# Kernel tuning notes

Hardware: AMD Instinct MI355X
Metric: run time of the kernel (lower is better)

## Reference

```python
import jax, jax.numpy as jnp
import numpy as np

N_NODES = 100000
N_EDGES = 1600000
HIDDEN = 128
N_REL = 8


def setup_inputs() -> dict:
    key = jax.random.key(0)
    ks = jax.random.split(key, 12)
    s = 1.0 / np.sqrt(HIDDEN)
    inp = {
        "node_idx": jnp.arange(N_NODES, dtype=jnp.int32),
        "edge_index": jax.random.randint(ks[0], (2, N_EDGES), 0, N_NODES, dtype=jnp.int32),
        "edge_type": jax.random.randint(ks[1], (N_EDGES,), 0, N_REL, dtype=jnp.int32),
        "embedding": jax.random.normal(ks[2], (N_NODES, HIDDEN), jnp.float32),
        "W_rel_0": jax.random.normal(ks[3], (N_REL, HIDDEN, HIDDEN), jnp.float32) * s,
        "W_root_0": jax.random.normal(ks[4], (HIDDEN, HIDDEN), jnp.float32) * s,
        "b_0": jnp.zeros((HIDDEN,), jnp.float32),
        "W_rel_1": jax.random.normal(ks[5], (N_REL, HIDDEN, HIDDEN), jnp.float32) * s,
        "W_root_1": jax.random.normal(ks[6], (HIDDEN, HIDDEN), jnp.float32) * s,
        "b_1": jnp.zeros((HIDDEN,), jnp.float32),
    }
    return inp


def _rgcn_conv(x, src, dst, et, W_rel, W_root, b):
    # PyG RGCNConv: out_i = x_i @ W_root + b + sum_r mean_{j in N_r(i)} x_j @ W_r
    n = x.shape[0]
    r = W_rel.shape[0]
    # Transform all nodes by all relations once (R small), then gather per edge.
    x_all = jnp.einsum('nd,rdf->rnf', x, W_rel)          # [R, N, d]
    msg = x_all[et, src]                                  # [E, d]
    # per-(relation, dst) mean normalization
    seg = et * n + dst                                    # [E]
    deg = jax.ops.segment_sum(jnp.ones(et.shape, jnp.float32), seg, num_segments=r * n)
    norm = 1.0 / jnp.maximum(deg[seg], 1.0)               # [E]
    agg = jax.ops.segment_sum(msg * norm[:, None], dst, num_segments=n)  # [N, d]
    return agg + x @ W_root + b


def reference(node_idx, edge_index, edge_type, embedding,
              W_rel_0, W_root_0, b_0, W_rel_1, W_root_1, b_1):
    src, dst = edge_index[0], edge_index[1]
    x = embedding[node_idx]
    x = jax.nn.relu(_rgcn_conv(x, src, dst, edge_type, W_rel_0, W_root_0, b_0))
    x = jax.nn.relu(_rgcn_conv(x, src, dst, edge_type, W_rel_1, W_root_1, b_1))
    return x
```

## Files before the change

### kernel.cpp

```cpp
#include <hip/hip_runtime.h>
#include <hip/hip_bf16.h>

typedef short bf16x8 __attribute__((ext_vector_type(8)));
typedef float f32x4 __attribute__((ext_vector_type(4)));

constexpr int NN = 100000;
constexpr int NE = 1600000;
constexpr int HH = 128;
constexpr int NR = 8;
constexpr int NBIN = 782;
constexpr int CAPB = 6144;

__device__ __forceinline__ unsigned short f2bf(float f) {
    unsigned b = __float_as_uint(f);
    b += 0x7fffu + ((b >> 16) & 1u);
    return (unsigned short)(b >> 16);
}

__global__ void convertWX(const float* __restrict__ Wr0, const float* __restrict__ Wq0,
                          const float* __restrict__ Wr1, const float* __restrict__ Wq1,
                          unsigned short* __restrict__ Wt,
                          const int* __restrict__ node_idx,
                          const float* __restrict__ emb,
                          unsigned* __restrict__ xb32) {
    if (blockIdx.x < 1152) {
        int o = blockIdx.x * 256 + threadIdx.x;
        int L = o / 147456;
        int rem = o - L * 147456;
        int s = rem >> 14;
        int p = rem & 16383;
        int f = p >> 7;
        int d = p & 127;
        const float* Wq = L ? Wq1 : Wq0;
        const float* Wr = L ? Wr1 : Wr0;
        float v = (s == 0) ? Wq[d * 128 + f] : Wr[((s - 1) * 128 + d) * 128 + f];
        int cs = (d >> 3) ^ (f & 7);
        Wt[(o & ~127) | (cs << 3) | (d & 7)] = f2bf(v);
    } else {
        int i = (blockIdx.x - 1152) * 256 + threadIdx.x;
        if (i >= NN * 64) return;
        int n = i >> 6, dp = i & 63;
        int row = node_idx[n];
        float2 v = *((const float2*)(emb + (size_t)row * HH) + dp);
        xb32[(size_t)n * 64 + dp] = (unsigned)f2bf(v.x) | ((unsigned)f2bf(v.y) << 16);
    }
}

__global__ __launch_bounds__(256) void binCount(const int* __restrict__ edst,
                                                unsigned* __restrict__ binCounts) {
    __shared__ unsigned hist[NBIN];
    for (int i = threadIdx.x; i < NBIN; i += 256) hist[i] = 0;
    __syncthreads();
    int stride = gridDim.x * 256;
    for (int e = blockIdx.x * 256 + threadIdx.x; e < NE; e += stride)
        atomicAdd(&hist[((unsigned)edst[e]) >> 7], 1u);
    __syncthreads();
    for (int i = threadIdx.x; i < NBIN; i += 256)
        if (hist[i]) atomicAdd(&binCounts[i], hist[i]);
}

__global__ void binScan(const unsigned* __restrict__ binCounts,
                        unsigned* __restrict__ binStarts,
                        unsigned* __restrict__ binCursor) {
    __shared__ unsigned sh[1024];
    int tid = threadIdx.x;
    unsigned v = (tid < NBIN) ? binCounts[tid] : 0u;
    sh[tid] = v;
    __syncthreads();
    for (int ofs = 1; ofs < 1024; ofs <<= 1) {
        unsigned t = (tid >= ofs) ? sh[tid - ofs] : 0u;
        __syncthreads();
        sh[tid] += t;
        __syncthreads();
    }
    if (tid < NBIN) {
        unsigned s = sh[tid] - v;
        binStarts[tid] = s;
        binCursor[tid] = s;
    }
    if (tid == 0) binStarts[NBIN] = NE;
}

__global__ __launch_bounds__(256) void binScatter(
        const int* __restrict__ esrc, const int* __restrict__ edst,
        const int* __restrict__ etype, unsigned* __restrict__ binCursor,
        unsigned* __restrict__ binned) {
    __shared__ unsigned hist[NBIN];
    __shared__ unsigned cur[NBIN];
    for (int i = threadIdx.x; i < NBIN; i += 256) hist[i] = 0;
    __syncthreads();
    int per = (NE + gridDim.x - 1) / gridDim.x;
    int lo = blockIdx.x * per;
    int hi = lo + per; if (hi > NE) hi = NE;
    for (int e = lo + threadIdx.x; e < hi; e += 256)
        atomicAdd(&hist[((unsigned)edst[e]) >> 7], 1u);
    __syncthreads();
    for (int i = threadIdx.x; i < NBIN; i += 256) {
        unsigned c = hist[i];
        cur[i] = c ? atomicAdd(&binCursor[i], c) : 0u;
    }
    __syncthreads();
    for (int e = lo + threadIdx.x; e < hi; e += 256) {
        unsigned d = (unsigned)edst[e];
        unsigned b = d >> 7;
        unsigned pos = atomicAdd(&cur[b], 1u);
        binned[pos] = (unsigned)esrc[e] | (((unsigned)etype[e]) << 17) |
                      ((d & 127u) << 20);
    }
}

__global__ __launch_bounds__(256) void binSort(
        const unsigned* __restrict__ binStarts, const unsigned* __restrict__ binned,
        unsigned* __restrict__ epk, unsigned* __restrict__ starts) {
    __shared__ unsigned hist[1024];
    __shared__ unsigned scn[1024];
    __shared__ unsigned cnts[1024];
    __shared__ unsigned part[256];
    __shared__ unsigned buf[CAPB];
    __shared__ unsigned outb[CAPB];
    int bin = blockIdx.x;
    int tid = threadIdx.x;
    unsigned base = binStarts[bin];
    int cnt = (int)(binStarts[bin + 1] - base);

    for (int i = tid; i < 1024; i += 256) hist[i] = 0;
    __syncthreads();
    for (int i = tid; i < cnt; i += 256) {
        unsigned p = binned[base + i];
        if (i < CAPB) buf[i] = p;
        atomicAdd(&hist[(p >> 17) & 0x3ffu], 1u);
    }
    __syncthreads();
    unsigned h4[4], tsum = 0;
#pragma unroll
    for (int j = 0; j < 4; ++j) { h4[j] = hist[tid * 4 + j]; tsum += h4[j]; }
    part[tid] = tsum;
    __syncthreads();
    for (int ofs = 1; ofs < 256; ofs <<= 1) {
        unsigned t = (tid >= ofs) ? part[tid - ofs] : 0u;
        __syncthreads();
        part[tid] += t;
        __syncthreads();
    }
    unsigned run = part[tid] - tsum;
#pragma unroll
    for (int j = 0; j < 4; ++j) { scn[tid * 4 + j] = run; run += h4[j]; }
    __syncthreads();
    for (int i = tid; i < 1024; i += 256) {
        starts[(size_t)bin * 1024 + i] = base + scn[i];
        cnts[i] = hist[i];
        hist[i] = scn[i];
    }
    __syncthreads();
    if (cnt <= CAPB) {
        for (int i = tid; i < cnt; i += 256) {
            unsigned p = buf[i];
            unsigned key = (p >> 17) & 0x3ffu;
            unsigned pos = atomicAdd(&hist[key], 1u);
            unsigned deg = cnts[key]; if (deg > 4095u) deg = 4095u;
            outb[pos] = ((p & 0x1ffffu) << 3) | (key & 7u) | (deg << 20);
        }
        __syncthreads();
        for (int i = tid; i < cnt; i += 256) epk[base + i] = outb[i];
    } else {
        for (int i = tid; i < cnt; i += 256) {
            unsigned p = binned[base + i];
            unsigned key = (p >> 17) & 0x3ffu;
            unsigned pos = atomicAdd(&hist[key], 1u);
            unsigned deg = cnts[key]; if (deg > 4095u) deg = 4095u;
            epk[base + pos] = ((p & 0x1ffffu) << 3) | (key & 7u) | (deg << 20);
        }
    }
}

__global__ __launch_bounds__(512, 4) void bigGemm(const unsigned short* x,
                                                  const unsigned short* __restrict__ Wt,
                                                  unsigned* __restrict__ y32,
                                                  unsigned* root32) {
    typedef __attribute__((address_space(3))) unsigned lds_u32_t;
    typedef const __attribute__((address_space(1))) unsigned glb_u32_t;
    __shared__ __align__(16) unsigned short Bl[2][16384];
    __shared__ __align__(16) unsigned Tld[64 * 64];

    int tid = threadIdx.x;
    int wid = tid >> 6, lane = tid & 63;
    int quad = lane >> 4, l16 = lane & 15;
    int wr = wid >> 1, wc = wid & 1;
    int m0 = blockIdx.x * 128;
    int sw = l16 & 7;

    auto prefetch = [&](int s, int b) {
        const char* gs = (const char*)Wt + (size_t)s * 32768 + wid * 4096 + lane * 16;
        char* ls = (char*)&Bl[b][0] + wid * 4096;
#pragma unroll
        for (int j = 0; j < 4; ++j)
            __builtin_amdgcn_global_load_lds((glb_u32_t*)(const void*)(gs + j * 1024),
                                             (lds_u32_t*)(void*)(ls + j * 1024),
                                             16, 0, 0);
    };

    prefetch(0, 0);

    bf16x8 ax[2][4];
#pragma unroll
    for (int nt = 0; nt < 2; ++nt) {
        int node = m0 + wr * 32 + nt * 16 + l16;
        node = node < NN ? node : NN - 1;
        const unsigned short* rp = x + (size_t)node * HH + quad * 8;
#pragma unroll
        for (int kt = 0; kt < 4; ++kt)
            ax[nt][kt] = *(const bf16x8*)(rp + kt * 32);
    }
    __syncthreads();

    for (int s = 0; s < 9; ++s) {
        if (s < 8) prefetch(s + 1, (s + 1) & 1);
        const char* Bb = (const char*)&Bl[s & 1][0];

        f32x4 acc[2][4];
#pragma unroll
        for (int nt = 0; nt < 2; ++nt)
#pragma unroll
            for (int ft = 0; ft < 4; ++ft) acc[nt][ft] = (f32x4){0.f, 0.f, 0.f, 0.f};

#pragma unroll
        for (int kt = 0; kt < 4; ++kt) {
            bf16x8 bw[4];
#pragma unroll
            for (int ft = 0; ft < 4; ++ft) {
                int f = wc * 64 + ft * 16 + l16;
                bw[ft] = *(const bf16x8*)(Bb + f * 256 +
                                          (((kt * 4 + quad) ^ sw) << 4));
            }
#pragma unroll
            for (int nt = 0; nt < 2; ++nt)
#pragma unroll
                for (int ft = 0; ft < 4; ++ft)
                    acc[nt][ft] = __builtin_amdgcn_mfma_f32_16x16x32_bf16(
                        bw[ft], ax[nt][kt], acc[nt][ft], 0, 0, 0);
        }

#pragma unroll
        for (int h = 0; h < 2; ++h) {
            __syncthreads();
            if ((wr >> 1) == h) {
#pragma unroll
                for (int nt = 0; nt < 2; ++nt) {
                    int rT = (wr & 1) * 32 + nt * 16 + l16;
#pragma unroll
                    for (int ft = 0; ft < 4; ++ft) {
                        unsigned d0, d1;
                        asm("v_cvt_pk_bf16_f32 %0, %1, %2"
                            : "=v"(d0) : "v"(acc[nt][ft][0]), "v"(acc[nt][ft][1]));
                        asm("v_cvt_pk_bf16_f32 %0, %1, %2"
                            : "=v"(d1) : "v"(acc[nt][ft][2]), "v"(acc[nt][ft][3]));
                        int slot = wc * 16 + ft * 4 + quad;
                        *(uint2*)((char*)Tld + rT * 256 +
                                  ((slot ^ ((rT & 7) << 2)) << 3)) =
                            make_uint2(d0, d1);
                    }
                }
            }
            __syncthreads();
#pragma unroll
            for (int p = 0; p < 2; ++p) {
                int rT = p * 32 + wid * 4 + quad;
                uint4 v = *(const uint4*)((char*)Tld + rT * 256 +
                                          (((l16 * 2) ^ ((rT & 7) << 2)) << 3));
                int node = m0 + h * 64 + rT;
                if (node < NN) {
                    unsigned* dst = (s == 0) ? (root32 + (size_t)node * 64)
                                             : (y32 + ((size_t)node * 8 + (s - 1)) * 64);
                    *(uint4*)(dst + l16 * 4) = v;
                }
            }
        }
    }
}

__global__ __launch_bounds__(256) void scatterAgg(
        const unsigned* __restrict__ starts, const unsigned* __restrict__ epk,
        const unsigned* __restrict__ y32, const unsigned* root32,
        const float* __restrict__ bias,
        float* __restrict__ outF, unsigned* outB) {
    int node = blockIdx.x * 4 + (threadIdx.x >> 6);
    if (node >= NN) return;
    int lane = threadIdx.x & 63;

    unsigned s0 = starts[(size_t)node * 8];
    unsigned s1 = starts[(size_t)node * 8 + 8];
    int cnt = (int)__builtin_amdgcn_readfirstlane((int)(s1 - s0));

    float ax = 0.f, ay = 0.f;
    for (int c0 = 0; c0 < cnt; c0 += 64) {
        unsigned myE = s0 + (unsigned)c0 + (unsigned)lane;
        unsigned pk = (myE < s1) ? epk[myE] : 0u;
        int cend = cnt - c0;
        if (cend > 64) cend = 64;
        for (int base = 0; base < cend; base += 8) {
            int m = cend - base;
            if (m > 8) m = 8;
            int bix = base << 2;
            unsigned pj[8], qj[8];
#pragma unroll
            for (int j = 0; j < 8; ++j)
                pj[j] = (unsigned)__builtin_amdgcn_ds_bpermute(bix + (j << 2), (int)pk);
#pragma unroll
            for (int j = 0; j < 8; ++j)
                if (j < m) qj[j] = y32[((pj[j] & 0xFFFFFu) << 6) + (unsigned)lane];
#pragma unroll
            for (int j = 0; j < 8; ++j) {
                if (j < m) {
                    float nr = __builtin_amdgcn_rcpf((float)(pj[j] >> 20));
                    float lo = __uint_as_float(qj[j] << 16);
                    float hi = __uint_as_float(qj[j] & 0xffff0000u);
                    ax += lo * nr;
                    ay += hi * nr;
                }
            }
        }
    }

    unsigned r = root32[(size_t)node * 64 + lane];
    float2 bv = ((const float2*)bias)[lane];
    float ox = ax + __uint_as_float(r << 16) + bv.x;
    float oy = ay + __uint_as_float(r & 0xffff0000u) + bv.y;
    ox = ox > 0.f ? ox : 0.f;
    oy = oy > 0.f ? oy : 0.f;
    if (outF) {
        *(float2*)(outF + (size_t)node * HH + lane * 2) = make_float2(ox, oy);
    } else {
        outB[(size_t)node * 64 + lane] =
            (unsigned)f2bf(ox) | ((unsigned)f2bf(oy) << 16);
    }
}

extern "C" void kernel_launch(void* const* d_in, const int* in_sizes, int n_in,
                              void* d_out, int out_size, void* d_ws, size_t ws_size,
                              hipStream_t stream) {
    const int* node_idx = (const int*)d_in[0];
    const int* eidx     = (const int*)d_in[1];
    const int* etype    = (const int*)d_in[2];
    const float* emb    = (const float*)d_in[3];
    const float* Wr0    = (const float*)d_in[4];
    const float* Wq0    = (const float*)d_in[5];
    const float* b0     = (const float*)d_in[6];
    const float* Wr1    = (const float*)d_in[7];
    const float* Wq1    = (const float*)d_in[8];
    const float* b1     = (const float*)d_in[9];
    const int* esrc = eidx;
    const int* edst = eidx + NE;

    char* ws = (char*)d_ws;
    size_t off = 0;
    auto alloc = [&](size_t bytes) -> void* {
        void* p = ws + off;
        off = (off + bytes + 255) & ~(size_t)255;
        return p;
    };
    unsigned* binCounts = (unsigned*)alloc((size_t)NBIN * 4);
    unsigned* binStarts = (unsigned*)alloc((size_t)(NBIN + 1) * 4);
    unsigned* binCursor = (unsigned*)alloc((size_t)NBIN * 4);
    unsigned* starts    = (unsigned*)alloc((size_t)NBIN * 1024 * 4);
    unsigned* epk       = (unsigned*)alloc((size_t)NE * 4);
    unsigned* xb32      = (unsigned*)alloc((size_t)NN * 64 * 4);
    unsigned* y32       = (unsigned*)alloc((size_t)NN * 8 * 64 * 4);
    unsigned short* Wt  = (unsigned short*)alloc((size_t)2 * 9 * 16384 * 2);
    unsigned* binned = y32;
    (void)ws_size; (void)n_in; (void)in_sizes; (void)out_size;

    hipMemsetAsync(binCounts, 0, (size_t)NBIN * 4, stream);
    convertWX<<<1152 + (NN * 64 + 255) / 256, 256, 0, stream>>>(
        Wr0, Wq0, Wr1, Wq1, Wt, node_idx, emb, xb32);
    binCount<<<256, 256, 0, stream>>>(edst, binCounts);
    binScan<<<1, 1024, 0, stream>>>(binCounts, binStarts, binCursor);
    binScatter<<<128, 256, 0, stream>>>(esrc, edst, etype, binCursor, binned);
    binSort<<<NBIN, 256, 0, stream>>>(binStarts, binned, epk, starts);

    int nblk = (NN + 127) / 128;
    bigGemm<<<nblk, 512, 0, stream>>>((const unsigned short*)xb32, Wt, y32, xb32);
    scatterAgg<<<(NN + 3) / 4, 256, 0, stream>>>(starts, epk, y32, xb32, b0,
                                                 nullptr, xb32);
    bigGemm<<<nblk, 512, 0, stream>>>((const unsigned short*)xb32, Wt + 147456,
                                      y32, xb32);
    scatterAgg<<<(NN + 3) / 4, 256, 0, stream>>>(starts, epk, y32, xb32, b1,
                                                 (float*)d_out, nullptr);
}
```

Baseline: 504.2 us.

## Fuse RGCN layer into aggregate-then-transform kernel per node tile

Each layer now runs in a single kernel that, for a 64-node tile, gathers and mean-aggregates raw neighbour features per relation into LDS and then multiplies by that relation's weight with MFMA, accumulating root and all relations in registers. Bias and ReLU are applied in the epilogue. This removes the large per-node, per-relation transformed tensor and the separate scatter pass, cutting global traffic substantially. In exchange the gather is done per relation with a serial per-node loop that may be latency-bound or unbalanced, and occupancy is lower.

```diff
diff --git a/kernel.cpp b/kernel.cpp
--- a/kernel.cpp
+++ b/kernel.cpp
@@ -173,165 +173,202 @@
     }
 }
 
-__global__ __launch_bounds__(512, 4) void bigGemm(const unsigned short* x,
-                                                  const unsigned short* __restrict__ Wt,
-                                                  unsigned* __restrict__ y32,
-                                                  unsigned* root32) {
+template<int OUT32>
+__global__ __launch_bounds__(256, 2) void rgcnFused(
+        const unsigned* __restrict__ xin,
+        const unsigned short* __restrict__ Wt,
+        const unsigned* __restrict__ starts, const unsigned* __restrict__ epk,
+        const float* __restrict__ bias,
+        unsigned* __restrict__ outB, float* __restrict__ outF) {
     typedef __attribute__((address_space(3))) unsigned lds_u32_t;
     typedef const __attribute__((address_space(1))) unsigned glb_u32_t;
-    __shared__ __align__(16) unsigned short Bl[2][16384];
-    __shared__ __align__(16) unsigned Tld[64 * 64];
+    __shared__ __align__(16) unsigned short Wl[2][16384];
+    __shared__ __align__(16) unsigned Agg[4096];
 
     int tid = threadIdx.x;
     int wid = tid >> 6, lane = tid & 63;
     int quad = lane >> 4, l16 = lane & 15;
     int wr = wid >> 1, wc = wid & 1;
-    int m0 = blockIdx.x * 128;
+    int node0 = blockIdx.x * 64;
     int sw = l16 & 7;
 
     auto prefetch = [&](int s, int b) {
-        const char* gs = (const char*)Wt + (size_t)s * 32768 + wid * 4096 + lane * 16;
-        char* ls = (char*)&Bl[b][0] + wid * 4096;
-#pragma unroll
-        for (int j = 0; j < 4; ++j)
-            __builtin_amdgcn_global_load_lds((glb_u32_t*)(const void*)(gs + j * 1024),
-                                             (lds_u32_t*)(void*)(ls + j * 1024),
+        const char* gs = (const char*)Wt + (size_t)s * 32768 + wid * 1024 + lane * 16;
+        char* ls = (char*)&Wl[b][0] + wid * 1024;
+#pragma unroll
+        for (int j = 0; j < 8; ++j)
+            __builtin_amdgcn_global_load_lds((glb_u32_t*)(const void*)(gs + j * 4096),
+                                             (lds_u32_t*)(void*)(ls + j * 4096),
                                              16, 0, 0);
     };
 
     prefetch(0, 0);
 
-    bf16x8 ax[2][4];
-#pragma unroll
-    for (int nt = 0; nt < 2; ++nt) {
-        int node = m0 + wr * 32 + nt * 16 + l16;
-        node = node < NN ? node : NN - 1;
-        const unsigned short* rp = x + (size_t)node * HH + quad * 8;
-#pragma unroll
-        for (int kt = 0; kt < 4; ++kt)
-            ax[nt][kt] = *(const bf16x8*)(rp + kt * 32);
-    }
-    __syncthreads();
+    f32x4 acc[2][4];
+#pragma unroll
+    for (int nt = 0; nt < 2; ++nt)
+#pragma unroll
+        for (int ft = 0; ft < 4; ++ft) acc[nt][ft] = (f32x4){0.f, 0.f, 0.f, 0.f};
 
     for (int s = 0; s < 9; ++s) {
+        __syncthreads();
         if (s < 8) prefetch(s + 1, (s + 1) & 1);
-        const char* Bb = (const char*)&Bl[s & 1][0];
-
-        f32x4 acc[2][4];
-#pragma unroll
-        for (int nt = 0; nt < 2; ++nt)
-#pragma unroll
-            for (int ft = 0; ft < 4; ++ft) acc[nt][ft] = (f32x4){0.f, 0.f, 0.f, 0.f};
-
+
+        if (s == 0) {
+#pragma unroll
+            for (int p = 0; p < 4; ++p) {
+                int i = p * 16 + (tid >> 4);
+                int c = tid & 15;
+                int nd = node0 + i; nd = nd < NN ? nd : NN - 1;
+                uint4 v = *((const uint4*)(xin + (size_t)nd * 64) + c);
+                *(uint4*)((char*)Agg + i * 256 + ((c ^ (i & 7)) << 4)) = v;
+            }
+        } else {
+            int r = s - 1;
+            int ndl = node0 + wid * 16 + (lane & 15);
+            if (ndl > NN - 1) ndl = NN - 1;
+            unsigned bv = starts[(size_t)ndl * 8 + r + ((lane >> 4) & 1)];
+            unsigned s0a[16]; int da[16];
+#pragma unroll
+            for (int t = 0; t < 16; ++t) {
+                unsigned a = (unsigned)__builtin_amdgcn_readlane((int)bv, t);
+                unsigned b = (unsigned)__builtin_amdgcn_readlane((int)bv, t + 16);
+                s0a[t] = a; da[t] = (int)(b - a);
+            }
+            float axv[16], ayv[16];
+#pragma unroll
+            for (int t = 0; t < 16; ++t) { axv[t] = 0.f; ayv[t] = 0.f; }
+#pragma unroll
+            for (int j = 0; j < 4; ++j) {
+                unsigned qv[16];
+#pragma unroll
+                for (int t = 0; t < 16; ++t)
+                    if (j < da[t]) {
+                        unsigned pk = epk[s0a[t] + j];
+                        qv[t] = xin[(size_t)((pk >> 3) & 0x1ffffu) * 64 + lane];
+                    }
+#pragma unroll
+                for (int t = 0; t < 16; ++t)
+                    if (j < da[t]) {
+                        axv[t] += __uint_as_float(qv[t] << 16);
+                        ayv[t] += __uint_as_float(qv[t] & 0xffff0000u);
+                    }
+            }
+#pragma unroll
+            for (int t = 0; t < 16; ++t) {
+                int e1 = (int)s0a[t] + da[t];
+                for (int e = (int)s0a[t] + 4; e < e1; ++e) {
+                    unsigned pk = epk[e];
+                    unsigned q = xin[(size_t)((pk >> 3) & 0x1ffffu) * 64 + lane];
+                    axv[t] += __uint_as_float(q << 16);
+                    ayv[t] += __uint_as_float(q & 0xffff0000u);
+                }
+            }
+#pragma unroll
+            for (int t = 0; t < 16; ++t) {
+                float nrm = da[t] > 0 ? __builtin_amdgcn_rcpf((float)da[t]) : 0.f;
+                float lo = axv[t] * nrm, hi = ayv[t] * nrm;
+                unsigned dw;
+                asm("v_cvt_pk_bf16_f32 %0, %1, %2" : "=v"(dw) : "v"(lo), "v"(hi));
+                int i = wid * 16 + t;
+                *(unsigned*)((char*)Agg + i * 256 +
+                             ((((lane >> 2) ^ (t & 7)) << 4) | ((lane & 3) << 2))) = dw;
+            }
+        }
+        __syncthreads();
+
+        const char* Bb = (const char*)&Wl[s & 1][0];
+        const char* Ab = (const char*)Agg;
 #pragma unroll
         for (int kt = 0; kt < 4; ++kt) {
-            bf16x8 bw[4];
-#pragma unroll
-            for (int ft = 0; ft < 4; ++ft) {
-                int f = wc * 64 + ft * 16 + l16;
-                bw[ft] = *(const bf16x8*)(Bb + f * 256 +
+            bf16x8 bw[4], axx[2];
+#pragma unroll
+            for (int ft = 0; ft < 4; ++ft)
+                bw[ft] = *(const bf16x8*)(Bb + (wc * 64 + ft * 16 + l16) * 256 +
                                           (((kt * 4 + quad) ^ sw) << 4));
-            }
+#pragma unroll
+            for (int nt = 0; nt < 2; ++nt)
+                axx[nt] = *(const bf16x8*)(Ab + (wr * 32 + nt * 16 + l16) * 256 +
+                                           (((kt * 4 + quad) ^ sw) << 4));
 #pragma unroll
             for (int nt = 0; nt < 2; ++nt)
 #pragma unroll
                 for (int ft = 0; ft < 4; ++ft)
                     acc[nt][ft] = __builtin_amdgcn_mfma_f32_16x16x32_bf16(
-                        bw[ft], ax[nt][kt], acc[nt][ft], 0, 0, 0);
-        }
-
+                        bw[ft], axx[nt], acc[nt][ft], 0, 0, 0);
+        }
+    }
+
+    float bvv[4][4];
+#pragma unroll
+    for (int ft = 0; ft < 4; ++ft)
+#pragma unroll
+        for (int rg = 0; rg < 4; ++rg)
+            bvv[ft][rg] = bias[wc * 64 + ft * 16 + quad * 4 + rg];
+
+    if (!OUT32) {
+        __syncthreads();
+#pragma unroll
+        for (int nt = 0; nt < 2; ++nt) {
+            int rT = wr * 32 + nt * 16 + l16;
+#pragma unroll
+            for (int ft = 0; ft < 4; ++ft) {
+                float v0 = acc[nt][ft][0] + bvv[ft][0]; v0 = v0 > 0.f ? v0 : 0.f;
+                float v1 = acc[nt][ft][1] + bvv[ft][1]; v1 = v1 > 0.f ? v1 : 0.f;
+                float v2 = acc[nt][ft][2] + bvv[ft][2]; v2 = v2 > 0.f ? v2 : 0.f;
+                float v3 = acc[nt][ft][3] + bvv[ft][3]; v3 = v3 > 0.f ? v3 : 0.f;
+                unsigned d0, d1;
+                asm("v_cvt_pk_bf16_f32 %0, %1, %2" : "=v"(d0) : "v"(v0), "v"(v1));
+                asm("v_cvt_pk_bf16_f32 %0, %1, %2" : "=v"(d1) : "v"(v2), "v"(v3));
+                int slot = wc * 16 + ft * 4 + quad;
+                *(uint2*)((char*)Agg + rT * 256 +
+                          ((slot ^ ((rT & 7) << 2)) << 3)) = make_uint2(d0, d1);
+            }
+        }
+        __syncthreads();
+#pragma unroll
+        for (int pp = 0; pp < 4; ++pp) {
+            int idx = pp * 256 + tid;
+            int rT = idx >> 4, c16 = idx & 15;
+            uint4 v = *(const uint4*)((char*)Agg + rT * 256 +
+                                      (((c16 * 2) ^ ((rT & 7) << 2)) << 3));
+            int node = node0 + rT;
+            if (node < NN) *((uint4*)(outB + (size_t)node * 64) + c16) = v;
+        }
+    } else {
 #pragma unroll
         for (int h = 0; h < 2; ++h) {
             __syncthreads();
-            if ((wr >> 1) == h) {
+            if (wr == h) {
 #pragma unroll
                 for (int nt = 0; nt < 2; ++nt) {
-                    int rT = (wr & 1) * 32 + nt * 16 + l16;
+                    int rloc = nt * 16 + l16;
 #pragma unroll
                     for (int ft = 0; ft < 4; ++ft) {
-                        unsigned d0, d1;
-                        asm("v_cvt_pk_bf16_f32 %0, %1, %2"
-                            : "=v"(d0) : "v"(acc[nt][ft][0]), "v"(acc[nt][ft][1]));
-                        asm("v_cvt_pk_bf16_f32 %0, %1, %2"
-                            : "=v"(d1) : "v"(acc[nt][ft][2]), "v"(acc[nt][ft][3]));
-                        int slot = wc * 16 + ft * 4 + quad;
-                        *(uint2*)((char*)Tld + rT * 256 +
-                                  ((slot ^ ((rT & 7) << 2)) << 3)) =
-                            make_uint2(d0, d1);
+                        f32x4 v;
+#pragma unroll
+                        for (int rg = 0; rg < 4; ++rg) {
+                            float u = acc[nt][ft][rg] + bvv[ft][rg];
+                            v[rg] = u > 0.f ? u : 0.f;
+                        }
+                        int c32 = wc * 16 + ft * 4 + quad;
+                        *(f32x4*)((char*)Agg + rloc * 512 +
+                                  ((c32 ^ ((rloc & 7) << 2)) << 4)) = v;
                     }
                 }
             }
             __syncthreads();
 #pragma unroll
-            for (int p = 0; p < 2; ++p) {
-                int rT = p * 32 + wid * 4 + quad;
-                uint4 v = *(const uint4*)((char*)Tld + rT * 256 +
-                                          (((l16 * 2) ^ ((rT & 7) << 2)) << 3));
-                int node = m0 + h * 64 + rT;
-                if (node < NN) {
-                    unsigned* dst = (s == 0) ? (root32 + (size_t)node * 64)
-                                             : (y32 + ((size_t)node * 8 + (s - 1)) * 64);
-                    *(uint4*)(dst + l16 * 4) = v;
-                }
-            }
-        }
-    }
-}
-
-__global__ __launch_bounds__(256) void scatterAgg(
-        const unsigned* __restrict__ starts, const unsigned* __restrict__ epk,
-        const unsigned* __restrict__ y32, const unsigned* root32,
-        const float* __restrict__ bias,
-        float* __restrict__ outF, unsigned* outB) {
-    int node = blockIdx.x * 4 + (threadIdx.x >> 6);
-    if (node >= NN) return;
-    int lane = threadIdx.x & 63;
-
-    unsigned s0 = starts[(size_t)node * 8];
-    unsigned s1 = starts[(size_t)node * 8 + 8];
-    int cnt = (int)__builtin_amdgcn_readfirstlane((int)(s1 - s0));
-
-    float ax = 0.f, ay = 0.f;
-    for (int c0 = 0; c0 < cnt; c0 += 64) {
-        unsigned myE = s0 + (unsigned)c0 + (unsigned)lane;
-        unsigned pk = (myE < s1) ? epk[myE] : 0u;
-        int cend = cnt - c0;
-        if (cend > 64) cend = 64;
-        for (int base = 0; base < cend; base += 8) {
-            int m = cend - base;
-            if (m > 8) m = 8;
-            int bix = base << 2;
-            unsigned pj[8], qj[8];
-#pragma unroll
-            for (int j = 0; j < 8; ++j)
-                pj[j] = (unsigned)__builtin_amdgcn_ds_bpermute(bix + (j << 2), (int)pk);
-#pragma unroll
-            for (int j = 0; j < 8; ++j)
-                if (j < m) qj[j] = y32[((pj[j] & 0xFFFFFu) << 6) + (unsigned)lane];
-#pragma unroll
-            for (int j = 0; j < 8; ++j) {
-                if (j < m) {
-                    float nr = __builtin_amdgcn_rcpf((float)(pj[j] >> 20));
-                    float lo = __uint_as_float(qj[j] << 16);
-                    float hi = __uint_as_float(qj[j] & 0xffff0000u);
-                    ax += lo * nr;
-                    ay += hi * nr;
-                }
-            }
-        }
-    }
-
-    unsigned r = root32[(size_t)node * 64 + lane];
-    float2 bv = ((const float2*)bias)[lane];
-    float ox = ax + __uint_as_float(r << 16) + bv.x;
-    float oy = ay + __uint_as_float(r & 0xffff0000u) + bv.y;
-    ox = ox > 0.f ? ox : 0.f;
-    oy = oy > 0.f ? oy : 0.f;
-    if (outF) {
-        *(float2*)(outF + (size_t)node * HH + lane * 2) = make_float2(ox, oy);
-    } else {
-        outB[(size_t)node * 64 + lane] =
-            (unsigned)f2bf(ox) | ((unsigned)f2bf(oy) << 16);
+            for (int pp = 0; pp < 4; ++pp) {
+                int idx = pp * 256 + tid;
+                int rloc = idx >> 5, c32 = idx & 31;
+                f32x4 v = *(const f32x4*)((char*)Agg + rloc * 512 +
+                                          ((c32 ^ ((rloc & 7) << 2)) << 4));
+                int node = node0 + h * 32 + rloc;
+                if (node < NN)
+                    *(f32x4*)(outF + (size_t)node * HH + c32 * 4) = v;
+            }
+        }
     }
 }
 
@@ -363,26 +400,22 @@
     unsigned* binCursor = (unsigned*)alloc((size_t)NBIN * 4);
     unsigned* starts    = (unsigned*)alloc((size_t)NBIN * 1024 * 4);
     unsigned* epk       = (unsigned*)alloc((size_t)NE * 4);
-    unsigned* xb32      = (unsigned*)alloc((size_t)NN * 64 * 4);
-    unsigned* y32       = (unsigned*)alloc((size_t)NN * 8 * 64 * 4);
+    unsigned* xA        = (unsigned*)alloc((size_t)NN * 64 * 4);
+    unsigned* xB        = (unsigned*)alloc((size_t)NN * 64 * 4);
     unsigned short* Wt  = (unsigned short*)alloc((size_t)2 * 9 * 16384 * 2);
-    unsigned* binned = y32;
+    unsigned* binned    = (unsigned*)alloc((size_t)NE * 4);
     (void)ws_size; (void)n_in; (void)in_sizes; (void)out_size;
 
     hipMemsetAsync(binCounts, 0, (size_t)NBIN * 4, stream);
     convertWX<<<1152 + (NN * 64 + 255) / 256, 256, 0, stream>>>(
-        Wr0, Wq0, Wr1, Wq1, Wt, node_idx, emb, xb32);
+        Wr0, Wq0, Wr1, Wq1, Wt, node_idx, emb, xA);
     binCount<<<256, 256, 0, stream>>>(edst, binCounts);
     binScan<<<1, 1024, 0, stream>>>(binCounts, binStarts, binCursor);
     binScatter<<<128, 256, 0, stream>>>(esrc, edst, etype, binCursor, binned);
     binSort<<<NBIN, 256, 0, stream>>>(binStarts, binned, epk, starts);
 
-    int nblk = (NN + 127) / 128;
-    bigGemm<<<nblk, 512, 0, stream>>>((const unsigned short*)xb32, Wt, y32, xb32);
-    scatterAgg<<<(NN + 3) / 4, 256, 0, stream>>>(starts, epk, y32, xb32, b0,
-                                                 nullptr, xb32);
-    bigGemm<<<nblk, 512, 0, stream>>>((const unsigned short*)xb32, Wt + 147456,
-                                      y32, xb32);
-    scatterAgg<<<(NN + 3) / 4, 256, 0, stream>>>(starts, epk, y32, xb32, b1,
-                                                 (float*)d_out, nullptr);
-}
+    int nblk = (NN + 63) / 64;
+    rgcnFused<0><<<nblk, 256, 0, stream>>>(xA, Wt, starts, epk, b0, xB, nullptr);
+    rgcnFused<1><<<nblk, 256, 0, stream>>>(xB, Wt + 147456, starts, epk, b1,
+                                           nullptr, (float*)d_out);
+}
```

Measured after the change: 721.7 us. +43.2%, slower.
